# Performance work log

Hardware: AMD Instinct MI355X
Metric: run time of the kernel (lower is better)

Reference implementation:

```python
import jax, jax.numpy as jnp
import numpy as np

D = 1024
NH = 16
HD = D // NH  # 64

def setup_inputs() -> dict:
    key = jax.random.key(0)
    ks = jax.random.split(key, 6)
    s = 1.0 / np.sqrt(D)
    x = jax.random.normal(ks[0], (4, 2048, D), dtype=jnp.float32)
    Wq = jax.random.normal(ks[1], (D, D), dtype=jnp.float32) * s
    Wk = jax.random.normal(ks[2], (D, D), dtype=jnp.float32) * s
    Wv = jax.random.normal(ks[3], (D, D), dtype=jnp.float32) * s
    Wo = jax.random.normal(ks[4], (D, D), dtype=jnp.float32) * s
    bo = jnp.zeros((D,), dtype=jnp.float32)
    return {"x": x, "Wq": Wq, "Wk": Wk, "Wv": Wv, "Wo": Wo, "bo": bo}

def reference(x, Wq, Wk, Wv, Wo, bo):
    B, N, _ = x.shape
    # conv1d(kernel=1, no bias) == linear with weight [out, in]
    q = jnp.einsum('bnd,ed->bne', x, Wq).reshape(B, N, NH, HD)
    k = jnp.einsum('bnd,ed->bne', x, Wk).reshape(B, N, NH, HD)
    v = jnp.einsum('bnd,ed->bne', x, Wv).reshape(B, N, NH, HD)
    scores = jnp.einsum('bqhd,bkhd->bhqk', q, k) / jnp.sqrt(jnp.float32(HD))
    attn = jax.nn.softmax(scores, axis=-1)
    out = jnp.einsum('bhqk,bkhd->bqhd', attn, v).reshape(B, N, D)
    # out_proj: Linear(D, D)
    out = jnp.einsum('bnd,ed->bne', out, Wo) + bo
    return out
```

## Files before the change

### kernel.cpp

```cpp
#include <hip/hip_runtime.h>
#include <stdint.h>

typedef unsigned short u16;
typedef __attribute__((__ext_vector_type__(4))) float f32x4;
typedef __attribute__((__ext_vector_type__(8))) __bf16 bf16x8;
typedef __attribute__((__ext_vector_type__(4))) unsigned short u16x4;
typedef __attribute__((__ext_vector_type__(8))) unsigned short u16x8;

#define DEV static __device__ __forceinline__

DEV u16 f2b(float f) {
  union { float f; unsigned u; } v; v.f = f;
  unsigned r = v.u + 0x7FFFu + ((v.u >> 16) & 1u);
  return (u16)(r >> 16);
}

typedef const __attribute__((address_space(1))) void* gas_t;
typedef __attribute__((address_space(3))) void* las_t;

DEV void gl_lds16(const void* g, void* l) {
  __builtin_amdgcn_global_load_lds((gas_t)(uintptr_t)g, (las_t)(uint32_t)(uintptr_t)l,
                                   16, 0, 0);
}

__global__ void cvt4(const float* __restrict__ s, u16* __restrict__ d, int n4) {
  const int i = blockIdx.x * 256 + threadIdx.x;
  if (i >= n4) return;
  const float4 f = reinterpret_cast<const float4*>(s)[i];
  u16x4 o;
  o.x = f2b(f.x); o.y = f2b(f.y); o.z = f2b(f.z); o.w = f2b(f.w);
  reinterpret_cast<u16x4*>(d)[i] = o;
}

__global__ void cvtW(const float* __restrict__ Wq, const float* __restrict__ Wk,
                     const float* __restrict__ Wv, const float* __restrict__ Wo,
                     u16* __restrict__ Wqkv, u16* __restrict__ Wob) {
  const int bid = blockIdx.x, sel = bid >> 10;
  const int i = (bid & 1023) * 256 + threadIdx.x;
  const float* s = sel == 0 ? Wq : sel == 1 ? Wk : sel == 2 ? Wv : Wo;
  u16* d = (sel == 3) ? Wob : Wqkv + sel * 1048576;
  const float4 f = reinterpret_cast<const float4*>(s)[i];
  u16x4 o;
  o.x = f2b(f.x); o.y = f2b(f.y); o.z = f2b(f.z); o.w = f2b(f.w);
  reinterpret_cast<u16x4*>(d)[i] = o;
}

template<int MODE>
__global__ __launch_bounds__(256, 2) void gemm_bt(
    const u16* __restrict__ A, const u16* __restrict__ B, int K, int tiles_n,
    u16* __restrict__ Qo, u16* __restrict__ Ko, u16* __restrict__ Vo,
    float* __restrict__ Fo, const float* __restrict__ bias, int N)
{
  __shared__ u16 smem[24576];
  const int nwg = gridDim.x;
  const int bid = blockIdx.x;
  const int swz = (bid & 7) * (nwg >> 3) + (bid >> 3);
  const int tm = swz / tiles_n, tn = swz % tiles_n;
  const int tid = threadIdx.x, wid = tid >> 6, lane = tid & 63;
  const int wr = wid >> 1, wc = wid & 1;
  const int lr = lane & 15, lk = lane >> 4;

  const f32x4 fz = {0.f, 0.f, 0.f, 0.f};
  f32x4 acc[4][4];
#pragma unroll
  for (int i = 0; i < 4; i++)
#pragma unroll
    for (int j = 0; j < 4; j++) acc[i][j] = fz;

  const u16* Ab = A + (size_t)tm * 128 * K;
  const u16* Bb = B + (size_t)tn * 128 * K;

  const int ca = tid, cb2 = tid + 256;
  const int ra = ca >> 2,  ka = ((ca  & 3) ^ ((ra  >> 1) & 3)) * 8;
  const int rb = cb2 >> 2, kb = ((cb2 & 3) ^ ((rb  >> 1) & 3)) * 8;

  auto stage = [&](int k0, int buf) {
    u16* As = smem + buf * 8192;
    u16* Bs = As + 4096;
    gl_lds16(Ab + (size_t)ra * K + k0 + ka, &As[wid * 512]);
    gl_lds16(Ab + (size_t)rb * K + k0 + kb, &As[2048 + wid * 512]);
    gl_lds16(Bb + (size_t)ra * K + k0 + ka, &Bs[wid * 512]);
    gl_lds16(Bb + (size_t)rb * K + k0 + kb, &Bs[2048 + wid * 512]);
  };

  const int nk = K >> 5;
  stage(0, 0);
  stage(32, 1);
  for (int t = 0; t < nk; t++) {
    const int cur = t % 3;
    if (t < nk - 1) asm volatile("s_waitcnt vmcnt(4)" ::: "memory");
    else            asm volatile("s_waitcnt vmcnt(0)" ::: "memory");
    asm volatile("s_barrier" ::: "memory");
    if (t + 2 < nk) stage((t + 2) * 32, (t + 2) % 3);
    const u16* As = smem + cur * 8192;
    const u16* Bs = As + 4096;
    bf16x8 af[4], bf[4];
#pragma unroll
    for (int i = 0; i < 4; i++) {
      const int row = wr * 64 + i * 16 + lr;
      af[i] = *reinterpret_cast<const bf16x8*>(&As[row * 32 + (lk ^ ((row >> 1) & 3)) * 8]);
    }
#pragma unroll
    for (int j = 0; j < 4; j++) {
      const int row = wc * 64 + j * 16 + lr;
      bf[j] = *reinterpret_cast<const bf16x8*>(&Bs[row * 32 + (lk ^ ((row >> 1) & 3)) * 8]);
    }
#pragma unroll
    for (int i = 0; i < 4; i++)
#pragma unroll
      for (int j = 0; j < 4; j++)
        acc[i][j] = __builtin_amdgcn_mfma_f32_16x16x32_bf16(af[i], bf[j], acc[i][j], 0, 0, 0);
  }

  const int row0 = tm * 128 + wr * 64;
  if constexpr (MODE == 0) {
    const int mat = (tn * 128) >> 10;
    if (mat < 2) {
      u16* Mo = (mat == 0) ? Qo : Ko;
      const float qs = (mat == 0) ? 0.18033688f : 1.0f;
#pragma unroll
      for (int i = 0; i < 4; i++) {
#pragma unroll
        for (int j = 0; j < 4; j++) {
          const int e0 = tn * 128 + wc * 64 + j * 16;
          const int h = (e0 & 1023) >> 6;
          const int d = (e0 & 63) + lr;
#pragma unroll
          for (int r = 0; r < 4; r++) {
            const int m = row0 + i * 16 + lk * 4 + r;
            const int bb = m >> 11, n = m & 2047;
            Mo[((bb * 16 + h) * 2048 + n) * 64 + d] = f2b(acc[i][j][r] * qs);
          }
        }
      }
    } else {
      __syncthreads();
#pragma unroll
      for (int i = 0; i < 4; i++) {
#pragma unroll
        for (int j = 0; j < 4; j++) {
          const int e = wc * 64 + j * 16 + lr;
          const int m4 = wr * 64 + i * 16 + lk * 4;
          u16x4 pk;
#pragma unroll
          for (int r = 0; r < 4; r++) pk[r] = f2b(acc[i][j][r]);
          *reinterpret_cast<u16x4*>(&smem[e * 128 + (m4 ^ ((e & 7) << 3))]) = pk;
        }
      }
      __syncthreads();
      const int e = tid >> 1, half = tid & 1;
      const int ch = tn * 128 + e;
      const int hh = (ch >> 6) & 15, d = ch & 63;
      const int bb = (tm * 128) >> 11, n0 = (tm * 128) & 2047;
      u16* Vrow = Vo + ((size_t)((bb * 16 + hh) * 64 + d)) * 2048 + n0 + half * 64;
      const int xe = (e & 7) << 3;
#pragma unroll
      for (int s = 0; s < 8; s++) {
        const int npl = half * 64 + s * 8;
        const int nA = (npl & ~31) | ((npl >> 1) & 12);
        const u16x4 a = *reinterpret_cast<const u16x4*>(&smem[e * 128 + (nA ^ xe)]);
        const u16x4 b = *reinterpret_cast<const u16x4*>(&smem[e * 128 + ((nA + 16) ^ xe)]);
        u16x8 o;
#pragma unroll
        for (int r = 0; r < 4; r++) { o[r] = a[r]; o[4 + r] = b[r]; }
        *reinterpret_cast<u16x8*>(&Vrow[s * 8]) = o;
      }
    }
  } else {
#pragma unroll
    for (int i = 0; i < 4; i++) {
#pragma unroll
      for (int j = 0; j < 4; j++) {
        const int col = tn * 128 + wc * 64 + j * 16 + lr;
        const float bv = bias[col];
#pragma unroll
        for (int r = 0; r < 4; r++) {
          const int m = row0 + i * 16 + lk * 4 + r;
          Fo[(size_t)m * N + col] = acc[i][j][r] + bv;
        }
      }
    }
  }
}

__global__ __launch_bounds__(256, 2) void attn_fwd(
    const u16* __restrict__ Q, const u16* __restrict__ K, const u16* __restrict__ Vt,
    u16* __restrict__ O)
{
  __shared__ u16 Ks[2][64 * 64];
  __shared__ u16 Vs[2][64 * 64];
  const int bh = blockIdx.x >> 4, qt = blockIdx.x & 15;
  const int tid = threadIdx.x, w = tid >> 6, lane = tid & 63;
  const int lr = lane & 15, lk = lane >> 4;
  const u16* Qp = Q + ((size_t)bh * 2048 + qt * 128) * 64;
  const u16* Kp = K + (size_t)bh * 2048 * 64;
  const u16* Vp = Vt + (size_t)bh * 64 * 2048;

  bf16x8 qfr[2][2];
#pragma unroll
  for (int qf = 0; qf < 2; qf++)
#pragma unroll
    for (int kk = 0; kk < 2; kk++)
      qfr[qf][kk] = *reinterpret_cast<const bf16x8*>(
          &Qp[(w * 32 + qf * 16 + lr) * 64 + kk * 32 + lk * 8]);

  const f32x4 fz = {0.f, 0.f, 0.f, 0.f};
  f32x4 oacc[2][4];
  float ls[2] = {0.f, 0.f};
#pragma unroll
  for (int qf = 0; qf < 2; qf++)
#pragma unroll
    for (int df = 0; df < 4; df++) oacc[qf][df] = fz;

  auto stage = [&](int kt, int buf) {
#pragma unroll
    for (int i = 0; i < 2; i++) {
      const int c = tid + 256 * i;
      const int r = c >> 3, ss = ((c & 7) ^ (r & 7)) * 8;
      gl_lds16(Kp + (size_t)(kt * 64 + r) * 64 + ss, &Ks[buf][w * 512 + i * 2048]);
      gl_lds16(Vp + (size_t)r * 2048 + kt * 64 + ss, &Vs[buf][w * 512 + i * 2048]);
    }
  };

  stage(0, 0);
  for (int kt = 0; kt < 32; kt++) {
    const int cur = kt & 1;
    asm volatile("s_waitcnt vmcnt(0)" ::: "memory");
    __syncthreads();
    if (kt < 31) stage(kt + 1, cur ^ 1);

    f32x4 sacc[2][4];
#pragma unroll
    for (int qf = 0; qf < 2; qf++)
#pragma unroll
      for (int kf = 0; kf < 4; kf++) sacc[qf][kf] = fz;
#pragma unroll
    for (int kk = 0; kk < 2; kk++) {
#pragma unroll
      for (int kf = 0; kf < 4; kf++) {
        const int row = kf * 16 + lr;
        bf16x8 kfr = *reinterpret_cast<const bf16x8*>(
            &Ks[cur][row * 64 + (((kk * 4 + lk) ^ (row & 7)) * 8)]);
        sacc[0][kf] = __builtin_amdgcn_mfma_f32_16x16x32_bf16(kfr, qfr[0][kk], sacc[0][kf], 0, 0, 0);
        sacc[1][kf] = __builtin_amdgcn_mfma_f32_16x16x32_bf16(kfr, qfr[1][kk], sacc[1][kf], 0, 0, 0);
      }
    }

    bf16x8 pa[2][2];
#pragma unroll
    for (int qf = 0; qf < 2; qf++) {
      float lsum = 0.f;
#pragma unroll
      for (int kf = 0; kf < 4; kf++)
#pragma unroll
        for (int r = 0; r < 4; r++) {
          const float pv = __builtin_amdgcn_exp2f(sacc[qf][kf][r]);
          sacc[qf][kf][r] = pv;
          lsum += pv;
        }
      ls[qf] += lsum;
#pragma unroll
      for (int kk = 0; kk < 2; kk++)
#pragma unroll
        for (int j = 0; j < 4; j++) {
          pa[qf][kk][j]     = (__bf16)sacc[qf][2 * kk][j];
          pa[qf][kk][4 + j] = (__bf16)sacc[qf][2 * kk + 1][j];
        }
    }

#pragma unroll
    for (int df = 0; df < 4; df++) {
      const int d = df * 16 + lr;
#pragma unroll
      for (int kk = 0; kk < 2; kk++) {
        bf16x8 vfr = *reinterpret_cast<const bf16x8*>(
            &Vs[cur][d * 64 + (((kk * 4 + lk) ^ (d & 7)) * 8)]);
        oacc[0][df] = __builtin_amdgcn_mfma_f32_16x16x32_bf16(pa[0][kk], vfr, oacc[0][df], 0, 0, 0);
        oacc[1][df] = __builtin_amdgcn_mfma_f32_16x16x32_bf16(pa[1][kk], vfr, oacc[1][df], 0, 0, 0);
      }
    }
  }

  const int b = bh >> 4, h = bh & 15;
#pragma unroll
  for (int qf = 0; qf < 2; qf++) {
    float l = ls[qf];
    l += __shfl_xor(l, 16);
    l += __shfl_xor(l, 32);
    const float linv = 1.f / l;
    float iv[4];
#pragma unroll
    for (int r = 0; r < 4; r++) iv[r] = __shfl(linv, lk * 4 + r);
#pragma unroll
    for (int df = 0; df < 4; df++)
#pragma unroll
      for (int r = 0; r < 4; r++) {
        const int n = qt * 128 + w * 32 + qf * 16 + lk * 4 + r;
        O[((size_t)b * 2048 + n) * 1024 + h * 64 + df * 16 + lr] =
            f2b(oacc[qf][df][r] * iv[r]);
      }
  }
}

extern "C" void kernel_launch(void* const* d_in, const int* in_sizes, int n_in,
                              void* d_out, int out_size, void* d_ws, size_t ws_size,
                              hipStream_t stream) {
  const float* x  = (const float*)d_in[0];
  const float* Wq = (const float*)d_in[1];
  const float* Wk = (const float*)d_in[2];
  const float* Wv = (const float*)d_in[3];
  const float* Wo = (const float*)d_in[4];
  const float* bo = (const float*)d_in[5];
  float* out = (float*)d_out;

  u16* ws   = (u16*)d_ws;
  u16* xb   = ws;
  u16* Wqkv = xb + 8388608;
  u16* Wob  = Wqkv + 3145728;
  u16* Qb   = Wob + 1048576;
  u16* Kb   = Qb + 8388608;
  u16* Vtb  = Kb + 8388608;

  cvt4<<<8192, 256, 0, stream>>>(x, xb, 2097152);
  cvtW<<<4096, 256, 0, stream>>>(Wq, Wk, Wv, Wo, Wqkv, Wob);

  gemm_bt<0><<<64 * 24, 256, 0, stream>>>(xb, Wqkv, 1024, 24,
                                          Qb, Kb, Vtb, nullptr, nullptr, 3072);
  attn_fwd<<<1024, 256, 0, stream>>>(Qb, Kb, Vtb, xb);
  gemm_bt<1><<<64 * 8, 256, 0, stream>>>(xb, Wob, 1024, 8,
                                         nullptr, nullptr, nullptr, out, bo, 1024);
}
```

Baseline: 180.1 us.

## Use 256x256-tile 512-thread QKV GEMM with deeper prefetch and MFMA priority

Replaces the 128x128 QKV projection GEMM with a dedicated 256x256-tile kernel of 8 waves. It uses 64-wide K stages, keeps two stages in flight with a partial vmcnt wait, and raises wave priority around MFMA blocks. The larger tile is meant to raise operand reuse and cut global traffic per flop, and setprio is also added around the attention kernel's MFMA sections. The cost is 128KB of LDS and heavy register use per block, and only 384 blocks, which may lower occupancy and leave some CUs idle.

```diff
diff --git a/kernel.cpp b/kernel.cpp
--- a/kernel.cpp
+++ b/kernel.cpp
@@ -45,10 +45,131 @@
   reinterpret_cast<u16x4*>(d)[i] = o;
 }
 
-template<int MODE>
-__global__ __launch_bounds__(256, 2) void gemm_bt(
+__global__ __launch_bounds__(512, 2) void gemm256(
+    const u16* __restrict__ A, const u16* __restrict__ B,
+    u16* __restrict__ Qo, u16* __restrict__ Ko, u16* __restrict__ Vo)
+{
+  __shared__ u16 smem[65536];
+  const int K = 1024;
+  const int nwg = gridDim.x;
+  const int bid = blockIdx.x;
+  const int swz = (bid & 7) * (nwg >> 3) + (bid >> 3);
+  const int tm = swz / 12, tn = swz % 12;
+  const int tid = threadIdx.x, wid = tid >> 6, lane = tid & 63;
+  const int wm = wid >> 2, wn = wid & 3;
+  const int lr = lane & 15, lk = lane >> 4;
+
+  const f32x4 fz = {0.f, 0.f, 0.f, 0.f};
+  f32x4 acc[8][4];
+#pragma unroll
+  for (int i = 0; i < 8; i++)
+#pragma unroll
+    for (int j = 0; j < 4; j++) acc[i][j] = fz;
+
+  const u16* Ab = A + (size_t)tm * 256 * K;
+  const u16* Bb = B + (size_t)tn * 256 * K;
+
+  auto stage = [&](int kt, int buf) {
+    u16* As = smem + buf * 32768;
+    u16* Bs = As + 16384;
+#pragma unroll
+    for (int i = 0; i < 4; i++) {
+      const int c = tid + 512 * i;
+      const int r = c >> 3;
+      const int col = kt * 64 + (((c & 7) ^ (r & 7)) * 8);
+      u16* dstA = &As[(i * 512 + wid * 64) * 8];
+      u16* dstB = &Bs[(i * 512 + wid * 64) * 8];
+      gl_lds16(Ab + (size_t)r * K + col, dstA);
+      gl_lds16(Bb + (size_t)r * K + col, dstB);
+    }
+  };
+
+  stage(0, 0);
+  stage(1, 1);
+  for (int T = 0; T < 16; T++) {
+    if (T < 15) asm volatile("s_waitcnt vmcnt(8)" ::: "memory");
+    else        asm volatile("s_waitcnt vmcnt(0)" ::: "memory");
+    asm volatile("s_barrier" ::: "memory");
+    const u16* As = smem + (T & 1) * 32768;
+    const u16* Bs = As + 16384;
+#pragma unroll
+    for (int ks = 0; ks < 2; ks++) {
+      bf16x8 af[8];
+#pragma unroll
+      for (int mf = 0; mf < 8; mf++) {
+        const int row = wm * 128 + mf * 16 + lr;
+        af[mf] = *reinterpret_cast<const bf16x8*>(
+            &As[row * 64 + (((ks * 4 + lk) ^ (row & 7)) * 8)]);
+      }
+#pragma unroll
+      for (int nf = 0; nf < 4; nf++) {
+        const int row = wn * 64 + nf * 16 + lr;
+        const bf16x8 bfr = *reinterpret_cast<const bf16x8*>(
+            &Bs[row * 64 + (((ks * 4 + lk) ^ (row & 7)) * 8)]);
+        __builtin_amdgcn_s_setprio(1);
+#pragma unroll
+        for (int mf = 0; mf < 8; mf++)
+          acc[mf][nf] = __builtin_amdgcn_mfma_f32_16x16x32_bf16(af[mf], bfr, acc[mf][nf], 0, 0, 0);
+        __builtin_amdgcn_s_setprio(0);
+      }
+    }
+    asm volatile("s_barrier" ::: "memory");
+    if (T + 2 < 16) stage(T + 2, T & 1);
+  }
+
+  const int mat = tn >> 2;
+  const int b = tm >> 3, n0 = (tm & 7) * 256;
+  if (mat < 2) {
+    u16* Mo = (mat == 0) ? Qo : Ko;
+    const float qs = (mat == 0) ? 0.18033688f : 1.0f;
+#pragma unroll
+    for (int mf = 0; mf < 8; mf++) {
+#pragma unroll
+      for (int nf = 0; nf < 4; nf++) {
+        const int e = (tn & 3) * 256 + wn * 64 + nf * 16 + lr;
+        const int h = e >> 6, d = e & 63;
+#pragma unroll
+        for (int r = 0; r < 4; r++) {
+          const int n = n0 + wm * 128 + mf * 16 + lk * 4 + r;
+          Mo[((b * 16 + h) * 2048 + n) * 64 + d] = f2b(acc[mf][nf][r] * qs);
+        }
+      }
+    }
+  } else {
+    __syncthreads();
+#pragma unroll
+    for (int mf = 0; mf < 8; mf++) {
+#pragma unroll
+      for (int nf = 0; nf < 4; nf++) {
+        const int e = wn * 64 + nf * 16 + lr;
+        const int m4 = wm * 128 + mf * 16 + lk * 4;
+        u16x4 pk;
+#pragma unroll
+        for (int r = 0; r < 4; r++) pk[r] = f2b(acc[mf][nf][r]);
+        *reinterpret_cast<u16x4*>(&smem[e * 256 + (m4 ^ ((e & 7) << 3))]) = pk;
+      }
+    }
+    __syncthreads();
+    const int e = tid >> 1, half = tid & 1;
+    const int h = ((tn & 3) << 2) + (e >> 6), d = e & 63;
+    u16* Vrow = Vo + ((size_t)((b * 16 + h) * 64 + d)) * 2048 + n0;
+    const int xe = (e & 7) << 3;
+#pragma unroll
+    for (int s = 0; s < 16; s++) {
+      const int npl = half * 128 + s * 8;
+      const int nA = (npl & ~31) | ((npl >> 1) & 12);
+      const u16x4 a = *reinterpret_cast<const u16x4*>(&smem[e * 256 + (nA ^ xe)]);
+      const u16x4 bq = *reinterpret_cast<const u16x4*>(&smem[e * 256 + ((nA + 16) ^ xe)]);
+      u16x8 o;
+#pragma unroll
+      for (int r = 0; r < 4; r++) { o[r] = a[r]; o[4 + r] = bq[r]; }
+      *reinterpret_cast<u16x8*>(&Vrow[npl]) = o;
+    }
+  }
+}
+
+__global__ __launch_bounds__(256, 2) void gemm_out(
     const u16* __restrict__ A, const u16* __restrict__ B, int K, int tiles_n,
-    u16* __restrict__ Qo, u16* __restrict__ Ko, u16* __restrict__ Vo,
     float* __restrict__ Fo, const float* __restrict__ bias, int N)
 {
   __shared__ u16 smem[24576];
@@ -113,71 +234,16 @@
   }
 
   const int row0 = tm * 128 + wr * 64;
-  if constexpr (MODE == 0) {
-    const int mat = (tn * 128) >> 10;
-    if (mat < 2) {
-      u16* Mo = (mat == 0) ? Qo : Ko;
-      const float qs = (mat == 0) ? 0.18033688f : 1.0f;
-#pragma unroll
-      for (int i = 0; i < 4; i++) {
-#pragma unroll
-        for (int j = 0; j < 4; j++) {
-          const int e0 = tn * 128 + wc * 64 + j * 16;
-          const int h = (e0 & 1023) >> 6;
-          const int d = (e0 & 63) + lr;
-#pragma unroll
-          for (int r = 0; r < 4; r++) {
-            const int m = row0 + i * 16 + lk * 4 + r;
-            const int bb = m >> 11, n = m & 2047;
-            Mo[((bb * 16 + h) * 2048 + n) * 64 + d] = f2b(acc[i][j][r] * qs);
-          }
-        }
-      }
-    } else {
-      __syncthreads();
-#pragma unroll
-      for (int i = 0; i < 4; i++) {
-#pragma unroll
-        for (int j = 0; j < 4; j++) {
-          const int e = wc * 64 + j * 16 + lr;
-          const int m4 = wr * 64 + i * 16 + lk * 4;
-          u16x4 pk;
-#pragma unroll
-          for (int r = 0; r < 4; r++) pk[r] = f2b(acc[i][j][r]);
-          *reinterpret_cast<u16x4*>(&smem[e * 128 + (m4 ^ ((e & 7) << 3))]) = pk;
-        }
-      }
-      __syncthreads();
-      const int e = tid >> 1, half = tid & 1;
-      const int ch = tn * 128 + e;
-      const int hh = (ch >> 6) & 15, d = ch & 63;
-      const int bb = (tm * 128) >> 11, n0 = (tm * 128) & 2047;
-      u16* Vrow = Vo + ((size_t)((bb * 16 + hh) * 64 + d)) * 2048 + n0 + half * 64;
-      const int xe = (e & 7) << 3;
-#pragma unroll
-      for (int s = 0; s < 8; s++) {
-        const int npl = half * 64 + s * 8;
-        const int nA = (npl & ~31) | ((npl >> 1) & 12);
-        const u16x4 a = *reinterpret_cast<const u16x4*>(&smem[e * 128 + (nA ^ xe)]);
-        const u16x4 b = *reinterpret_cast<const u16x4*>(&smem[e * 128 + ((nA + 16) ^ xe)]);
-        u16x8 o;
-#pragma unroll
-        for (int r = 0; r < 4; r++) { o[r] = a[r]; o[4 + r] = b[r]; }
-        *reinterpret_cast<u16x8*>(&Vrow[s * 8]) = o;
-      }
-    }
-  } else {
-#pragma unroll
-    for (int i = 0; i < 4; i++) {
-#pragma unroll
-      for (int j = 0; j < 4; j++) {
-        const int col = tn * 128 + wc * 64 + j * 16 + lr;
-        const float bv = bias[col];
-#pragma unroll
-        for (int r = 0; r < 4; r++) {
-          const int m = row0 + i * 16 + lk * 4 + r;
-          Fo[(size_t)m * N + col] = acc[i][j][r] + bv;
-        }
+#pragma unroll
+  for (int i = 0; i < 4; i++) {
+#pragma unroll
+    for (int j = 0; j < 4; j++) {
+      const int col = tn * 128 + wc * 64 + j * 16 + lr;
+      const float bv = bias[col];
+#pragma unroll
+      for (int r = 0; r < 4; r++) {
+        const int m = row0 + i * 16 + lk * 4 + r;
+        Fo[(size_t)m * N + col] = acc[i][j][r] + bv;
       }
     }
   }
@@ -234,6 +300,7 @@
     for (int qf = 0; qf < 2; qf++)
 #pragma unroll
       for (int kf = 0; kf < 4; kf++) sacc[qf][kf] = fz;
+    __builtin_amdgcn_s_setprio(1);
 #pragma unroll
     for (int kk = 0; kk < 2; kk++) {
 #pragma unroll
@@ -245,6 +312,7 @@
         sacc[1][kf] = __builtin_amdgcn_mfma_f32_16x16x32_bf16(kfr, qfr[1][kk], sacc[1][kf], 0, 0, 0);
       }
     }
+    __builtin_amdgcn_s_setprio(0);
 
     bf16x8 pa[2][2];
 #pragma unroll
@@ -268,6 +336,7 @@
         }
     }
 
+    __builtin_amdgcn_s_setprio(1);
 #pragma unroll
     for (int df = 0; df < 4; df++) {
       const int d = df * 16 + lr;
@@ -279,6 +348,7 @@
         oacc[1][df] = __builtin_amdgcn_mfma_f32_16x16x32_bf16(pa[1][kk], vfr, oacc[1][df], 0, 0, 0);
       }
     }
+    __builtin_amdgcn_s_setprio(0);
   }
 
   const int b = bh >> 4, h = bh & 15;
@@ -324,9 +394,7 @@
   cvt4<<<8192, 256, 0, stream>>>(x, xb, 2097152);
   cvtW<<<4096, 256, 0, stream>>>(Wq, Wk, Wv, Wo, Wqkv, Wob);
 
-  gemm_bt<0><<<64 * 24, 256, 0, stream>>>(xb, Wqkv, 1024, 24,
-                                          Qb, Kb, Vtb, nullptr, nullptr, 3072);
+  gemm256<<<384, 512, 0, stream>>>(xb, Wqkv, Qb, Kb, Vtb);
   attn_fwd<<<1024, 256, 0, stream>>>(Qb, Kb, Vtb, xb);
-  gemm_bt<1><<<64 * 8, 256, 0, stream>>>(xb, Wob, 1024, 8,
-                                         nullptr, nullptr, nullptr, out, bo, 1024);
-}
+  gemm_out<<<64 * 8, 256, 0, stream>>>(xb, Wob, 1024, 8, out, bo, 1024);
+}
```

Result: no change. 182.2 us (+1.2%).
